# Kernel optimization log

Hardware: AMD Instinct MI355X
Metric: run time of the kernel (lower is better)

Reference implementation:

```python
import jax, jax.numpy as jnp
import numpy as np

MARGIN = 0.3
BIG = jnp.float32(1e30)  # finite sentinel for masked max/min (avoids inf-inf NaNs)


def setup_inputs() -> dict:
    key = jax.random.key(0)
    k1, k2 = jax.random.split(key)
    B, D, N_CLASSES = 8192, 256, 512
    embeddings = jax.random.normal(k1, (B, D), dtype=jnp.float32)
    labels = jax.random.randint(k2, (B,), 0, N_CLASSES, dtype=jnp.int64)
    return {"embeddings": embeddings, "labels": labels}


def reference(embeddings, labels):
    B = embeddings.shape[0]
    # pairwise squared L2 distances via Gram matrix
    dot = embeddings @ embeddings.T                      # [B, B]
    sq = jnp.diagonal(dot)[:, None]                      # [B, 1]
    dist2 = jnp.maximum(sq + sq.T - 2.0 * dot, 0.0)      # [B, B]

    labels_eq = labels[:, None] == labels[None, :]       # [B, B]
    eye = jnp.eye(B, dtype=bool)
    pos_mask = labels_eq & ~eye                          # positives, excluding self
    neg_mask = ~labels_eq

    has_pos = jnp.any(pos_mask, axis=1)                  # rows contributing to loss
    # hardest positive per anchor: masked max
    d_ap = jnp.max(jnp.where(pos_mask, dist2, -BIG), axis=1)  # [B]

    # semi-hard negatives: d_ap < d < d_ap + margin
    semi_hard = neg_mask & (dist2 > d_ap[:, None]) & (dist2 < d_ap[:, None] + MARGIN)
    has_semi = jnp.any(semi_hard, axis=1)
    final_neg = jnp.where(has_semi[:, None], semi_hard, neg_mask)  # fallback to all negatives
    d_an = jnp.min(jnp.where(final_neg, dist2, BIG), axis=1)       # [B]

    per_row = jax.nn.relu(d_ap - d_an + MARGIN)          # [B]
    per_row = jnp.where(has_pos, per_row, 0.0)
    n_valid = jnp.maximum(jnp.sum(has_pos), 1)
    return jnp.sum(per_row) / n_valid.astype(per_row.dtype)
```

## Files before the change

### kernel.cpp

```cpp
#include <hip/hip_runtime.h>

#define MARGIN 0.3f
#define BIGF 1e30f
#define MAXC 64

constexpr int D = 256;

typedef __attribute__((ext_vector_type(8))) _Float16 f16x8;
typedef __attribute__((ext_vector_type(4))) _Float16 f16x4;
typedef __attribute__((ext_vector_type(4))) float f32x4;

__device__ __forceinline__ void gll16(const void* g, void* l) {
  __builtin_amdgcn_global_load_lds(
      (const __attribute__((address_space(1))) unsigned int*)g,
      (__attribute__((address_space(3))) unsigned int*)l, 16, 0, 0);
}

#define SCB() __builtin_amdgcn_sched_barrier(0)
#define BAR() __builtin_amdgcn_s_barrier()
#define WAITV(N) asm volatile("s_waitcnt vmcnt(" #N ")" ::: "memory")

__global__ __launch_bounds__(256)
void k0_prep(const float* __restrict__ E, const int* __restrict__ labels,
             _Float16* __restrict__ H, float* __restrict__ sq,
             unsigned* __restrict__ minAll, unsigned* __restrict__ minAb,
             int* __restrict__ cnt, int* __restrict__ members, int B) {
  int wave = threadIdx.x >> 6, lane = threadIdx.x & 63;
  int row = blockIdx.x * 4 + wave;
  if (row >= B) return;
  float4 v = *(const float4*)&E[(size_t)row * D + lane * 4];
  f16x4 h;
  h.x = (_Float16)v.x; h.y = (_Float16)v.y;
  h.z = (_Float16)v.z; h.w = (_Float16)v.w;
  {
    const int panel = row >> 8, r = row & 255;
    const int kt = lane >> 3;
    const int cc = (lane >> 1) & 3;
    const int slot = cc ^ ((r >> 1) & 3);
    const size_t off = ((size_t)(panel * 8 + kt) * 256 + r) * 32 + slot * 8 + (lane & 1) * 4;
    *(f16x4*)&H[off] = h;
  }
  float s = v.x * v.x + v.y * v.y + v.z * v.z + v.w * v.w;
#pragma unroll
  for (int off = 32; off; off >>= 1) s += __shfl_xor(s, off);
  if (lane == 0) {
    sq[row] = s;
    minAll[row] = __float_as_uint(BIGF);
    minAb[row] = __float_as_uint(BIGF);
    int lab = labels[row];
    int p = atomicAdd(&cnt[lab], 1);
    if (p < MAXC) members[lab * MAXC + p] = row;
  }
}

__global__ __launch_bounds__(256)
void k1_dap(const float* __restrict__ E, const int* __restrict__ labels,
            const float* __restrict__ sq, const int* __restrict__ cnt,
            const int* __restrict__ members, float* __restrict__ d_ap,
            int* __restrict__ haspos, int B) {
  int wave = threadIdx.x >> 6, lane = threadIdx.x & 63;
  int i = blockIdx.x * 4 + wave;
  if (i >= B) return;
  float4 a = *(const float4*)&E[(size_t)i * D + lane * 4];
  int li = labels[i];
  int n = min(cnt[li], MAXC);
  float sqi = sq[i];
  float m = -BIGF;
  const int* mem = &members[li * MAXC];
  int p = 0;
  for (; p + 3 < n; p += 4) {
    int j0 = mem[p], j1 = mem[p + 1], j2 = mem[p + 2], j3 = mem[p + 3];
    float4 b0 = *(const float4*)&E[(size_t)j0 * D + lane * 4];
    float4 b1 = *(const float4*)&E[(size_t)j1 * D + lane * 4];
    float4 b2 = *(const float4*)&E[(size_t)j2 * D + lane * 4];
    float4 b3 = *(const float4*)&E[(size_t)j3 * D + lane * 4];
    float s0 = a.x * b0.x + a.y * b0.y + a.z * b0.z + a.w * b0.w;
    float s1 = a.x * b1.x + a.y * b1.y + a.z * b1.z + a.w * b1.w;
    float s2 = a.x * b2.x + a.y * b2.y + a.z * b2.z + a.w * b2.w;
    float s3 = a.x * b3.x + a.y * b3.y + a.z * b3.z + a.w * b3.w;
#pragma unroll
    for (int off = 32; off; off >>= 1) {
      s0 += __shfl_xor(s0, off);
      s1 += __shfl_xor(s1, off);
      s2 += __shfl_xor(s2, off);
      s3 += __shfl_xor(s3, off);
    }
    float d0 = fmaxf(sqi + sq[j0] - 2.f * s0, 0.f);
    float d1 = fmaxf(sqi + sq[j1] - 2.f * s1, 0.f);
    float d2 = fmaxf(sqi + sq[j2] - 2.f * s2, 0.f);
    float d3 = fmaxf(sqi + sq[j3] - 2.f * s3, 0.f);
    if (j0 != i) m = fmaxf(m, d0);
    if (j1 != i) m = fmaxf(m, d1);
    if (j2 != i) m = fmaxf(m, d2);
    if (j3 != i) m = fmaxf(m, d3);
  }
  for (; p < n; ++p) {
    int j = mem[p];
    if (j == i) continue;
    float4 b = *(const float4*)&E[(size_t)j * D + lane * 4];
    float s = a.x * b.x + a.y * b.y + a.z * b.z + a.w * b.w;
#pragma unroll
    for (int off = 32; off; off >>= 1) s += __shfl_xor(s, off);
    m = fmaxf(m, fmaxf(sqi + sq[j] - 2.f * s, 0.f));
  }
  if (lane == 0) {
    d_ap[i] = (n > 1) ? m : -BIGF;
    haspos[i] = (n > 1) ? 1 : 0;
  }
}

__global__ __launch_bounds__(256, 4)
void k2_f16(const _Float16* __restrict__ H, const float* __restrict__ sq,
            const float* __restrict__ d_ap, const int* __restrict__ labels,
            unsigned* __restrict__ minAll, unsigned* __restrict__ minAb, int T) {
  __shared__ __align__(16) unsigned char smem[32768];
  __shared__ float sqI[128], sqJ[128], dapI[128], dapJ[128];
  __shared__ int labI[128], labJ[128];
  __shared__ unsigned smAJ[128], smBJ[128];

  const int tid = threadIdx.x;
  const int lane = tid & 63;
  const int wave = tid >> 6;
  const int wr = wave >> 1, wc = wave & 1;
  const int lo4 = lane & 15, hi4 = lane >> 4;

  const int nwg = gridDim.x;
  const int bid = blockIdx.x;
  const int swz = ((nwg & 7) == 0) ? (bid & 7) * (nwg >> 3) + (bid >> 3) : bid;
  int ti = (int)((sqrtf(8.f * (float)swz + 1.f) - 1.f) * 0.5f);
  while ((ti + 1) * (ti + 2) / 2 <= swz) ++ti;
  while (ti * (ti + 1) / 2 > swz) --ti;
  const int tj = swz - ti * (ti + 1) / 2;
  const int iBase = ti * 128, jBase = tj * 128;
  const bool offdiag = (ti != tj);

  const _Float16* HA = H + (size_t)(ti >> 1) * 8 * 8192 + (size_t)(ti & 1) * 4096;
  const _Float16* HB = H + (size_t)(tj >> 1) * 8 * 8192 + (size_t)(tj & 1) * 4096;
  const int f0 = tid, f1 = 256 + tid;

  auto STAGE = [&](int buf, int kt) {
    unsigned char* base = smem + buf * 16384;
    const _Float16* sa = HA + (size_t)kt * 8192;
    const _Float16* sb = HB + (size_t)kt * 8192;
    gll16(sa + f0 * 8, base + f0 * 16);
    gll16(sa + f1 * 8, base + f1 * 16);
    gll16(sb + f0 * 8, base + 8192 + f0 * 16);
    gll16(sb + f1 * 8, base + 8192 + f1 * 16);
  };

  f32x4 acc[4][4];
#pragma unroll
  for (int m = 0; m < 4; ++m)
#pragma unroll
    for (int n = 0; n < 4; ++n) acc[m][n] = (f32x4){0.f, 0.f, 0.f, 0.f};

  const int pc = hi4 ^ ((lo4 >> 1) & 3);

  auto COMPUTE = [&](int buf) {
    const _Float16* Ab = (const _Float16*)(smem + buf * 16384);
    const _Float16* Bb = Ab + 4096;
    f16x8 aF[4], bF[4];
#pragma unroll
    for (int m = 0; m < 4; ++m)
      aF[m] = *(const f16x8*)(Ab + (wr * 64 + m * 16 + lo4) * 32 + pc * 8);
#pragma unroll
    for (int n = 0; n < 4; ++n)
      bF[n] = *(const f16x8*)(Bb + (wc * 64 + n * 16 + lo4) * 32 + pc * 8);
    __builtin_amdgcn_s_setprio(1);
#pragma unroll
    for (int m = 0; m < 4; ++m)
#pragma unroll
      for (int n = 0; n < 4; ++n)
        acc[m][n] = __builtin_amdgcn_mfma_f32_16x16x32_f16(aF[m], bF[n], acc[m][n], 0, 0, 0);
    __builtin_amdgcn_s_setprio(0);
  };

  STAGE(0, 0);
  STAGE(1, 1);
  if (tid < 128) {
    int gi = iBase + tid;
    sqI[tid] = sq[gi]; labI[tid] = labels[gi]; dapI[tid] = d_ap[gi];
  } else {
    int t = tid - 128;
    int gj = jBase + t;
    sqJ[t] = sq[gj]; labJ[t] = labels[gj]; dapJ[t] = d_ap[gj];
    smAJ[t] = smBJ[t] = __float_as_uint(BIGF);
  }
  __syncthreads();
  COMPUTE(0); SCB(); BAR(); SCB(); STAGE(0, 2);
  WAITV(4); SCB(); BAR(); SCB(); COMPUTE(1); SCB(); BAR(); SCB(); STAGE(1, 3);
  WAITV(4); SCB(); BAR(); SCB(); COMPUTE(0); SCB(); BAR(); SCB(); STAGE(0, 4);
  WAITV(4); SCB(); BAR(); SCB(); COMPUTE(1); SCB(); BAR(); SCB(); STAGE(1, 5);
  WAITV(4); SCB(); BAR(); SCB(); COMPUTE(0); SCB(); BAR(); SCB(); STAGE(0, 6);
  WAITV(4); SCB(); BAR(); SCB(); COMPUTE(1); SCB(); BAR(); SCB(); STAGE(1, 7);
  WAITV(4); SCB(); BAR(); SCB(); COMPUTE(0); SCB(); BAR(); SCB();
  WAITV(0); SCB(); BAR(); SCB(); COMPUTE(1);
  __syncthreads();

  unsigned* scr = (unsigned*)smem;
#pragma unroll
  for (int s = 0; s < 20; ++s) scr[s * 256 + tid] = 0xFFFFFFFFu;
  __syncthreads();

  float sjv[4], djv[4];
  int ljv[4];
#pragma unroll
  for (int n = 0; n < 4; ++n) {
    int lj = wc * 64 + n * 16 + lo4;
    sjv[n] = sqJ[lj]; djv[n] = dapJ[lj]; ljv[n] = labJ[lj];
  }
  float cA[4], cB[4];
#pragma unroll
  for (int n = 0; n < 4; ++n) { cA[n] = BIGF; cB[n] = BIGF; }

#pragma unroll
  for (int m = 0; m < 4; ++m) {
#pragma unroll
    for (int reg = 0; reg < 4; ++reg) {
      const int li = wr * 64 + m * 16 + hi4 * 4 + reg;
      const float si = sqI[li], da = dapI[li];
      const int lbi = labI[li];
      float rA = BIGF, rB = BIGF;
#pragma unroll
      for (int n = 0; n < 4; ++n) {
        float dd = fmaxf(fmaf(-2.f, acc[m][n][reg], si + sjv[n]), 0.f);
        float ddm = (ljv[n] != lbi) ? dd : BIGF;
        rA = fminf(rA, ddm);
        rB = fminf(rB, (ddm > da) ? ddm : BIGF);
        if (offdiag) {
          cA[n] = fminf(cA[n], ddm);
          cB[n] = fminf(cB[n], (ddm > djv[n]) ? ddm : BIGF);
        }
      }
      atomicMin(&scr[li * 20 + lo4], __float_as_uint(rA));
      atomicMin(&scr[2560 + li * 20 + lo4], __float_as_uint(rB));
    }
  }
  if (offdiag) {
#pragma unroll
    for (int n = 0; n < 4; ++n) {
      const int lj = wc * 64 + n * 16 + lo4;
      float a = cA[n], b = cB[n];
      a = fminf(a, __shfl_xor(a, 16)); b = fminf(b, __shfl_xor(b, 16));
      a = fminf(a, __shfl_xor(a, 32)); b = fminf(b, __shfl_xor(b, 32));
      if (hi4 == 0) {
        atomicMin(&smAJ[lj], __float_as_uint(a));
        atomicMin(&smBJ[lj], __float_as_uint(b));
      }
    }
  }
  __syncthreads();

  {
    const int q = tid >> 7, i = tid & 127;
    const uint4* p4 = (const uint4*)&scr[q * 2560 + i * 20];
    uint4 a = p4[0], b = p4[1], c = p4[2], d4 = p4[3];
    unsigned u = min(min(min(a.x, a.y), min(a.z, a.w)),
                     min(min(min(b.x, b.y), min(b.z, b.w)),
                         min(min(min(c.x, c.y), min(c.z, c.w)),
                             min(min(d4.x, d4.y), min(d4.z, d4.w)))));
    unsigned* dst = q ? minAb : minAll;
    atomicMin(&dst[iBase + i], u);
    if (offdiag) {
      unsigned w = q ? smBJ[i] : smAJ[i];
      atomicMin(&dst[jBase + i], w);
    }
  }
}

__global__ __launch_bounds__(1024)
void k3_final(const float* __restrict__ d_ap, const int* __restrict__ haspos,
              const unsigned* __restrict__ minAll, const unsigned* __restrict__ minAb,
              float* __restrict__ out, int B) {
  __shared__ float ssum[1024];
  __shared__ int scnt[1024];
  int t = threadIdx.x;
  float lsum = 0.f;
  int lcnt = 0;
  for (int i = t; i < B; i += 1024) {
    float mA = __uint_as_float(minAll[i]);
    float mB = __uint_as_float(minAb[i]);
    float dap = d_ap[i];
    float dan = (mB < dap + MARGIN) ? mB : mA;
    float loss = fmaxf(dap - dan + MARGIN, 0.f);
    if (haspos[i]) { lsum += loss; lcnt += 1; }
  }
  ssum[t] = lsum;
  scnt[t] = lcnt;
  __syncthreads();
  for (int off = 512; off; off >>= 1) {
    if (t < off) { ssum[t] += ssum[t + off]; scnt[t] += scnt[t + off]; }
    __syncthreads();
  }
  if (t == 0) out[0] = ssum[0] / (float)max(scnt[0], 1);
}

extern "C" void kernel_launch(void* const* d_in, const int* in_sizes, int n_in,
                              void* d_out, int out_size, void* d_ws, size_t ws_size,
                              hipStream_t stream) {
  const float* E = (const float*)d_in[0];
  const int* labels = (const int*)d_in[1];
  int B = in_sizes[1];

  float* ws = (float*)d_ws;
  float* sq = ws;
  float* dap = ws + B;
  int* haspos = (int*)(ws + 2 * B);
  unsigned* minAll = (unsigned*)(ws + 3 * B);
  unsigned* minAb = (unsigned*)(ws + 4 * B);
  int* cnt = (int*)(ws + 5 * B);
  int* members = cnt + 512;
  _Float16* H = (_Float16*)(members + 512 * MAXC);
  float* out = (float*)d_out;

  hipMemsetAsync(cnt, 0, 512 * sizeof(int), stream);
  k0_prep<<<(B + 3) / 4, 256, 0, stream>>>(E, labels, H, sq, minAll, minAb, cnt, members, B);
  k1_dap<<<(B + 3) / 4, 256, 0, stream>>>(E, labels, sq, cnt, members, dap, haspos, B);
  int T = B / 128;
  int nwg = T * (T + 1) / 2;
  k2_f16<<<nwg, 256, 0, stream>>>(H, sq, dap, labels, minAll, minAb, T);
  k3_final<<<1, 1024, 0, stream>>>(dap, haspos, minAll, minAb, out, B);
}
```

Measured before the change: 78.96 us.

## Replace 4-wave 128x128 Gram tiles with single-wave 64x64 tiles, no barriers

The pairwise-distance kernel now uses one 64-lane wave per workgroup, each handling a 64x64 tile of the upper-triangular Gram matrix instead of four waves sharing a 128x128 tile. With a single wave, all workgroup barriers are removed. Per-row metadata (sq, d_ap, labels) is read straight from global memory, and column minima go directly to global atomics instead of through shared staging. This removes barrier stalls and gives the scheduler many more small workgroups. In exchange, each tile reuses less data, so global fp16 loads and global atomic traffic roughly double.

```diff
diff --git a/kernel.cpp b/kernel.cpp
--- a/kernel.cpp
+++ b/kernel.cpp
@@ -17,8 +17,6 @@
 }
 
 #define SCB() __builtin_amdgcn_sched_barrier(0)
-#define BAR() __builtin_amdgcn_s_barrier()
-#define WAITV(N) asm volatile("s_waitcnt vmcnt(" #N ")" ::: "memory")
 
 __global__ __launch_bounds__(256)
 void k0_prep(const float* __restrict__ E, const int* __restrict__ labels,
@@ -109,19 +107,13 @@
   }
 }
 
-__global__ __launch_bounds__(256, 4)
-void k2_f16(const _Float16* __restrict__ H, const float* __restrict__ sq,
-            const float* __restrict__ d_ap, const int* __restrict__ labels,
-            unsigned* __restrict__ minAll, unsigned* __restrict__ minAb, int T) {
-  __shared__ __align__(16) unsigned char smem[32768];
-  __shared__ float sqI[128], sqJ[128], dapI[128], dapJ[128];
-  __shared__ int labI[128], labJ[128];
-  __shared__ unsigned smAJ[128], smBJ[128];
-
-  const int tid = threadIdx.x;
-  const int lane = tid & 63;
-  const int wave = tid >> 6;
-  const int wr = wave >> 1, wc = wave & 1;
+__global__ __launch_bounds__(64)
+void k2_wave(const _Float16* __restrict__ H, const float* __restrict__ sq,
+             const float* __restrict__ d_ap, const int* __restrict__ labels,
+             unsigned* __restrict__ minAll, unsigned* __restrict__ minAb, int T) {
+  __shared__ __align__(16) _Float16 sm[2][4096];
+
+  const int lane = threadIdx.x;
   const int lo4 = lane & 15, hi4 = lane >> 4;
 
   const int nwg = gridDim.x;
@@ -131,21 +123,22 @@
   while ((ti + 1) * (ti + 2) / 2 <= swz) ++ti;
   while (ti * (ti + 1) / 2 > swz) --ti;
   const int tj = swz - ti * (ti + 1) / 2;
-  const int iBase = ti * 128, jBase = tj * 128;
+  const int iBase = ti * 64, jBase = tj * 64;
   const bool offdiag = (ti != tj);
 
-  const _Float16* HA = H + (size_t)(ti >> 1) * 8 * 8192 + (size_t)(ti & 1) * 4096;
-  const _Float16* HB = H + (size_t)(tj >> 1) * 8 * 8192 + (size_t)(tj & 1) * 4096;
-  const int f0 = tid, f1 = 256 + tid;
+  const _Float16* HA = H + (size_t)(ti >> 2) * 65536 + (size_t)(ti & 3) * 2048;
+  const _Float16* HB = H + (size_t)(tj >> 2) * 65536 + (size_t)(tj & 3) * 2048;
 
   auto STAGE = [&](int buf, int kt) {
-    unsigned char* base = smem + buf * 16384;
     const _Float16* sa = HA + (size_t)kt * 8192;
     const _Float16* sb = HB + (size_t)kt * 8192;
-    gll16(sa + f0 * 8, base + f0 * 16);
-    gll16(sa + f1 * 8, base + f1 * 16);
-    gll16(sb + f0 * 8, base + 8192 + f0 * 16);
-    gll16(sb + f1 * 8, base + 8192 + f1 * 16);
+    _Float16* la = &sm[buf][0] + lane * 8;
+    _Float16* lb = &sm[buf][2048] + lane * 8;
+#pragma unroll
+    for (int p = 0; p < 4; ++p) {
+      gll16(sa + p * 512 + lane * 8, la + p * 512);
+      gll16(sb + p * 512 + lane * 8, lb + p * 512);
+    }
   };
 
   f32x4 acc[4][4];
@@ -155,59 +148,53 @@
     for (int n = 0; n < 4; ++n) acc[m][n] = (f32x4){0.f, 0.f, 0.f, 0.f};
 
   const int pc = hi4 ^ ((lo4 >> 1) & 3);
-
-  auto COMPUTE = [&](int buf) {
-    const _Float16* Ab = (const _Float16*)(smem + buf * 16384);
-    const _Float16* Bb = Ab + 4096;
-    f16x8 aF[4], bF[4];
-#pragma unroll
-    for (int m = 0; m < 4; ++m)
-      aF[m] = *(const f16x8*)(Ab + (wr * 64 + m * 16 + lo4) * 32 + pc * 8);
-#pragma unroll
-    for (int n = 0; n < 4; ++n)
-      bF[n] = *(const f16x8*)(Bb + (wc * 64 + n * 16 + lo4) * 32 + pc * 8);
-    __builtin_amdgcn_s_setprio(1);
-#pragma unroll
-    for (int m = 0; m < 4; ++m)
-#pragma unroll
-      for (int n = 0; n < 4; ++n)
-        acc[m][n] = __builtin_amdgcn_mfma_f32_16x16x32_f16(aF[m], bF[n], acc[m][n], 0, 0, 0);
-    __builtin_amdgcn_s_setprio(0);
-  };
 
   STAGE(0, 0);
   STAGE(1, 1);
-  if (tid < 128) {
-    int gi = iBase + tid;
-    sqI[tid] = sq[gi]; labI[tid] = labels[gi]; dapI[tid] = d_ap[gi];
-  } else {
-    int t = tid - 128;
-    int gj = jBase + t;
-    sqJ[t] = sq[gj]; labJ[t] = labels[gj]; dapJ[t] = d_ap[gj];
-    smAJ[t] = smBJ[t] = __float_as_uint(BIGF);
-  }
-  __syncthreads();
-  COMPUTE(0); SCB(); BAR(); SCB(); STAGE(0, 2);
-  WAITV(4); SCB(); BAR(); SCB(); COMPUTE(1); SCB(); BAR(); SCB(); STAGE(1, 3);
-  WAITV(4); SCB(); BAR(); SCB(); COMPUTE(0); SCB(); BAR(); SCB(); STAGE(0, 4);
-  WAITV(4); SCB(); BAR(); SCB(); COMPUTE(1); SCB(); BAR(); SCB(); STAGE(1, 5);
-  WAITV(4); SCB(); BAR(); SCB(); COMPUTE(0); SCB(); BAR(); SCB(); STAGE(0, 6);
-  WAITV(4); SCB(); BAR(); SCB(); COMPUTE(1); SCB(); BAR(); SCB(); STAGE(1, 7);
-  WAITV(4); SCB(); BAR(); SCB(); COMPUTE(0); SCB(); BAR(); SCB();
-  WAITV(0); SCB(); BAR(); SCB(); COMPUTE(1);
-  __syncthreads();
-
-  unsigned* scr = (unsigned*)smem;
-#pragma unroll
-  for (int s = 0; s < 20; ++s) scr[s * 256 + tid] = 0xFFFFFFFFu;
-  __syncthreads();
+
+#define KSTEP(BUF, NKT, VMW, DOSTAGE)                                          \
+  {                                                                            \
+    asm volatile("s_waitcnt vmcnt(" VMW ")" ::: "memory");                     \
+    SCB();                                                                     \
+    const _Float16* Ab = &sm[BUF][0];                                          \
+    const _Float16* Bb = &sm[BUF][2048];                                       \
+    f16x8 aF[4], bF[4];                                                        \
+    _Pragma("unroll") for (int m = 0; m < 4; ++m)                              \
+        aF[m] = *(const f16x8*)(Ab + (m * 16 + lo4) * 32 + pc * 8);            \
+    _Pragma("unroll") for (int n = 0; n < 4; ++n)                              \
+        bF[n] = *(const f16x8*)(Bb + (n * 16 + lo4) * 32 + pc * 8);            \
+    asm volatile("s_waitcnt lgkmcnt(0)" ::: "memory");                         \
+    SCB();                                                                     \
+    if (DOSTAGE) STAGE(BUF, NKT);                                              \
+    __builtin_amdgcn_s_setprio(1);                                             \
+    _Pragma("unroll") for (int m = 0; m < 4; ++m)                              \
+        _Pragma("unroll") for (int n = 0; n < 4; ++n)                          \
+            acc[m][n] =                                                        \
+                __builtin_amdgcn_mfma_f32_16x16x32_f16(aF[m], bF[n],           \
+                                                       acc[m][n], 0, 0, 0);    \
+    __builtin_amdgcn_s_setprio(0);                                             \
+  }
+
+  KSTEP(0, 2, "8", true);
+  KSTEP(1, 3, "8", true);
+  KSTEP(0, 4, "8", true);
+  KSTEP(1, 5, "8", true);
+  KSTEP(0, 6, "8", true);
+  KSTEP(1, 7, "8", true);
+  KSTEP(0, 0, "8", false);
+  KSTEP(1, 0, "0", false);
+#undef KSTEP
+
+  unsigned* scr = (unsigned*)&sm[0][0];
+#pragma unroll
+  for (int s = 0; s < 40; ++s) scr[s * 64 + lane] = 0xFFFFFFFFu;
 
   float sjv[4], djv[4];
   int ljv[4];
 #pragma unroll
   for (int n = 0; n < 4; ++n) {
-    int lj = wc * 64 + n * 16 + lo4;
-    sjv[n] = sqJ[lj]; djv[n] = dapJ[lj]; ljv[n] = labJ[lj];
+    int gj = jBase + n * 16 + lo4;
+    sjv[n] = sq[gj]; djv[n] = d_ap[gj]; ljv[n] = labels[gj];
   }
   float cA[4], cB[4];
 #pragma unroll
@@ -217,9 +204,9 @@
   for (int m = 0; m < 4; ++m) {
 #pragma unroll
     for (int reg = 0; reg < 4; ++reg) {
-      const int li = wr * 64 + m * 16 + hi4 * 4 + reg;
-      const float si = sqI[li], da = dapI[li];
-      const int lbi = labI[li];
+      const int li = m * 16 + hi4 * 4 + reg;
+      const float si = sq[iBase + li], da = d_ap[iBase + li];
+      const int lbi = labels[iBase + li];
       float rA = BIGF, rB = BIGF;
 #pragma unroll
       for (int n = 0; n < 4; ++n) {
@@ -233,38 +220,34 @@
         }
       }
       atomicMin(&scr[li * 20 + lo4], __float_as_uint(rA));
-      atomicMin(&scr[2560 + li * 20 + lo4], __float_as_uint(rB));
+      atomicMin(&scr[1280 + li * 20 + lo4], __float_as_uint(rB));
     }
   }
   if (offdiag) {
 #pragma unroll
     for (int n = 0; n < 4; ++n) {
-      const int lj = wc * 64 + n * 16 + lo4;
       float a = cA[n], b = cB[n];
       a = fminf(a, __shfl_xor(a, 16)); b = fminf(b, __shfl_xor(b, 16));
       a = fminf(a, __shfl_xor(a, 32)); b = fminf(b, __shfl_xor(b, 32));
       if (hi4 == 0) {
-        atomicMin(&smAJ[lj], __float_as_uint(a));
-        atomicMin(&smBJ[lj], __float_as_uint(b));
+        int gj = jBase + n * 16 + lo4;
+        atomicMin(&minAll[gj], __float_as_uint(a));
+        atomicMin(&minAb[gj], __float_as_uint(b));
       }
     }
   }
-  __syncthreads();
-
-  {
-    const int q = tid >> 7, i = tid & 127;
-    const uint4* p4 = (const uint4*)&scr[q * 2560 + i * 20];
+#pragma unroll
+  for (int it = 0; it < 2; ++it) {
+    const int idx = it * 64 + lane;
+    const int q = idx >> 6, li = idx & 63;
+    const uint4* p4 = (const uint4*)&scr[q * 1280 + li * 20];
     uint4 a = p4[0], b = p4[1], c = p4[2], d4 = p4[3];
     unsigned u = min(min(min(a.x, a.y), min(a.z, a.w)),
                      min(min(min(b.x, b.y), min(b.z, b.w)),
                          min(min(min(c.x, c.y), min(c.z, c.w)),
                              min(min(d4.x, d4.y), min(d4.z, d4.w)))));
     unsigned* dst = q ? minAb : minAll;
-    atomicMin(&dst[iBase + i], u);
-    if (offdiag) {
-      unsigned w = q ? smBJ[i] : smAJ[i];
-      atomicMin(&dst[jBase + i], w);
-    }
+    atomicMin(&dst[iBase + li], u);
   }
 }
 
@@ -316,8 +299,8 @@
   hipMemsetAsync(cnt, 0, 512 * sizeof(int), stream);
   k0_prep<<<(B + 3) / 4, 256, 0, stream>>>(E, labels, H, sq, minAll, minAb, cnt, members, B);
   k1_dap<<<(B + 3) / 4, 256, 0, stream>>>(E, labels, sq, cnt, members, dap, haspos, B);
-  int T = B / 128;
+  int T = B / 64;
   int nwg = T * (T + 1) / 2;
-  k2_f16<<<nwg, 256, 0, stream>>>(H, sq, dap, labels, minAll, minAb, T);
+  k2_wave<<<nwg, 64, 0, stream>>>(H, sq, dap, labels, minAll, minAb, T);
   k3_final<<<1, 1024, 0, stream>>>(dap, haspos, minAll, minAb, out, B);
 }
```

Result: slower. 90.40 us (+14.5%).

## Triple-buffer GEMM staging and fuse final reduction via last-block ticket

Applied to the files above, without the earlier changes.

The k2 tile kernel moves from double to triple-buffered LDS staging with two k-steps of prefetch in flight, and lowers its occupancy hint from 4 to 3 blocks to fit the larger shared memory. The separate single-block final reduction kernel is removed. Its work now runs in whichever k2 block takes the last value of an atomic ticket counter, which saves a kernel launch and its tail. In exchange, every block pays an atomic and a threadfence, there is less occupancy, and the final reduction runs on a 256-thread block instead of 1024 threads.

```diff
diff --git a/kernel.cpp b/kernel.cpp
--- a/kernel.cpp
+++ b/kernel.cpp
@@ -109,14 +109,17 @@
   }
 }
 
-__global__ __launch_bounds__(256, 4)
+__global__ __launch_bounds__(256, 3)
 void k2_f16(const _Float16* __restrict__ H, const float* __restrict__ sq,
             const float* __restrict__ d_ap, const int* __restrict__ labels,
-            unsigned* __restrict__ minAll, unsigned* __restrict__ minAb, int T) {
-  __shared__ __align__(16) unsigned char smem[32768];
+            unsigned* __restrict__ minAll, unsigned* __restrict__ minAb,
+            const int* __restrict__ haspos, unsigned* __restrict__ ticket,
+            float* __restrict__ out, int T, int B) {
+  __shared__ __align__(16) _Float16 stg[3][8192];
   __shared__ float sqI[128], sqJ[128], dapI[128], dapJ[128];
   __shared__ int labI[128], labJ[128];
   __shared__ unsigned smAJ[128], smBJ[128];
+  __shared__ unsigned sdone;
 
   const int tid = threadIdx.x;
   const int lane = tid & 63;
@@ -134,12 +137,12 @@
   const int iBase = ti * 128, jBase = tj * 128;
   const bool offdiag = (ti != tj);
 
-  const _Float16* HA = H + (size_t)(ti >> 1) * 8 * 8192 + (size_t)(ti & 1) * 4096;
-  const _Float16* HB = H + (size_t)(tj >> 1) * 8 * 8192 + (size_t)(tj & 1) * 4096;
+  const _Float16* HA = H + (size_t)(ti >> 1) * 65536 + (size_t)(ti & 1) * 4096;
+  const _Float16* HB = H + (size_t)(tj >> 1) * 65536 + (size_t)(tj & 1) * 4096;
   const int f0 = tid, f1 = 256 + tid;
 
   auto STAGE = [&](int buf, int kt) {
-    unsigned char* base = smem + buf * 16384;
+    unsigned char* base = (unsigned char*)&stg[buf][0];
     const _Float16* sa = HA + (size_t)kt * 8192;
     const _Float16* sb = HB + (size_t)kt * 8192;
     gll16(sa + f0 * 8, base + f0 * 16);
@@ -157,7 +160,7 @@
   const int pc = hi4 ^ ((lo4 >> 1) & 3);
 
   auto COMPUTE = [&](int buf) {
-    const _Float16* Ab = (const _Float16*)(smem + buf * 16384);
+    const _Float16* Ab = &stg[buf][0];
     const _Float16* Bb = Ab + 4096;
     f16x8 aF[4], bF[4];
 #pragma unroll
@@ -177,6 +180,7 @@
 
   STAGE(0, 0);
   STAGE(1, 1);
+  STAGE(2, 2);
   if (tid < 128) {
     int gi = iBase + tid;
     sqI[tid] = sq[gi]; labI[tid] = labels[gi]; dapI[tid] = d_ap[gi];
@@ -187,17 +191,18 @@
     smAJ[t] = smBJ[t] = __float_as_uint(BIGF);
   }
   __syncthreads();
-  COMPUTE(0); SCB(); BAR(); SCB(); STAGE(0, 2);
-  WAITV(4); SCB(); BAR(); SCB(); COMPUTE(1); SCB(); BAR(); SCB(); STAGE(1, 3);
-  WAITV(4); SCB(); BAR(); SCB(); COMPUTE(0); SCB(); BAR(); SCB(); STAGE(0, 4);
-  WAITV(4); SCB(); BAR(); SCB(); COMPUTE(1); SCB(); BAR(); SCB(); STAGE(1, 5);
-  WAITV(4); SCB(); BAR(); SCB(); COMPUTE(0); SCB(); BAR(); SCB(); STAGE(0, 6);
-  WAITV(4); SCB(); BAR(); SCB(); COMPUTE(1); SCB(); BAR(); SCB(); STAGE(1, 7);
-  WAITV(4); SCB(); BAR(); SCB(); COMPUTE(0); SCB(); BAR(); SCB();
-  WAITV(0); SCB(); BAR(); SCB(); COMPUTE(1);
-  __syncthreads();
-
-  unsigned* scr = (unsigned*)smem;
+
+  COMPUTE(0); SCB(); BAR(); SCB(); STAGE(0, 3); WAITV(8); SCB(); BAR(); SCB();
+  COMPUTE(1); SCB(); BAR(); SCB(); STAGE(1, 4); WAITV(8); SCB(); BAR(); SCB();
+  COMPUTE(2); SCB(); BAR(); SCB(); STAGE(2, 5); WAITV(8); SCB(); BAR(); SCB();
+  COMPUTE(0); SCB(); BAR(); SCB(); STAGE(0, 6); WAITV(8); SCB(); BAR(); SCB();
+  COMPUTE(1); SCB(); BAR(); SCB(); STAGE(1, 7); WAITV(8); SCB(); BAR(); SCB();
+  COMPUTE(2); SCB(); BAR(); SCB(); WAITV(4); SCB(); BAR(); SCB();
+  COMPUTE(0); SCB(); BAR(); SCB(); WAITV(0); SCB(); BAR(); SCB();
+  COMPUTE(1);
+  __syncthreads();
+
+  unsigned* scr = (unsigned*)&stg[0][0];
 #pragma unroll
   for (int s = 0; s < 20; ++s) scr[s * 256 + tid] = 0xFFFFFFFFu;
   __syncthreads();
@@ -266,33 +271,38 @@
       atomicMin(&dst[jBase + i], w);
     }
   }
-}
-
-__global__ __launch_bounds__(1024)
-void k3_final(const float* __restrict__ d_ap, const int* __restrict__ haspos,
-              const unsigned* __restrict__ minAll, const unsigned* __restrict__ minAb,
-              float* __restrict__ out, int B) {
-  __shared__ float ssum[1024];
-  __shared__ int scnt[1024];
-  int t = threadIdx.x;
-  float lsum = 0.f;
-  int lcnt = 0;
-  for (int i = t; i < B; i += 1024) {
-    float mA = __uint_as_float(minAll[i]);
-    float mB = __uint_as_float(minAb[i]);
-    float dap = d_ap[i];
-    float dan = (mB < dap + MARGIN) ? mB : mA;
-    float loss = fmaxf(dap - dan + MARGIN, 0.f);
-    if (haspos[i]) { lsum += loss; lcnt += 1; }
-  }
-  ssum[t] = lsum;
-  scnt[t] = lcnt;
-  __syncthreads();
-  for (int off = 512; off; off >>= 1) {
-    if (t < off) { ssum[t] += ssum[t + off]; scnt[t] += scnt[t + off]; }
+
+  __syncthreads();
+  if (tid == 0) {
+    __threadfence();
+    sdone = atomicAdd(ticket, 1u);
+  }
+  __syncthreads();
+  if (sdone == (unsigned)(nwg - 1)) {
+    __threadfence();
+    float* rsum = (float*)&stg[2][0];
+    int* rcnt = (int*)(rsum + 256);
+    float lsum = 0.f;
+    int lcnt = 0;
+    for (int i = tid; i < B; i += 256) {
+      unsigned uA = atomicMin(&minAll[i], 0xFFFFFFFFu);
+      unsigned uB = atomicMin(&minAb[i], 0xFFFFFFFFu);
+      float mA = __uint_as_float(uA);
+      float mB = __uint_as_float(uB);
+      float dap = d_ap[i];
+      float dan = (mB < dap + MARGIN) ? mB : mA;
+      float loss = fmaxf(dap - dan + MARGIN, 0.f);
+      if (haspos[i]) { lsum += loss; lcnt += 1; }
+    }
+    rsum[tid] = lsum;
+    rcnt[tid] = lcnt;
     __syncthreads();
-  }
-  if (t == 0) out[0] = ssum[0] / (float)max(scnt[0], 1);
+    for (int off = 128; off; off >>= 1) {
+      if (tid < off) { rsum[tid] += rsum[tid + off]; rcnt[tid] += rcnt[tid + off]; }
+      __syncthreads();
+    }
+    if (tid == 0) out[0] = rsum[0] / (float)max(rcnt[0], 1);
+  }
 }
 
 extern "C" void kernel_launch(void* const* d_in, const int* in_sizes, int n_in,
@@ -309,15 +319,15 @@
   unsigned* minAll = (unsigned*)(ws + 3 * B);
   unsigned* minAb = (unsigned*)(ws + 4 * B);
   int* cnt = (int*)(ws + 5 * B);
-  int* members = cnt + 512;
+  unsigned* ticket = (unsigned*)(cnt + 512);
+  int* members = cnt + 516;
   _Float16* H = (_Float16*)(members + 512 * MAXC);
   float* out = (float*)d_out;
 
-  hipMemsetAsync(cnt, 0, 512 * sizeof(int), stream);
+  hipMemsetAsync(cnt, 0, 516 * sizeof(int), stream);
   k0_prep<<<(B + 3) / 4, 256, 0, stream>>>(E, labels, H, sq, minAll, minAb, cnt, members, B);
   k1_dap<<<(B + 3) / 4, 256, 0, stream>>>(E, labels, sq, cnt, members, dap, haspos, B);
   int T = B / 128;
   int nwg = T * (T + 1) / 2;
-  k2_f16<<<nwg, 256, 0, stream>>>(H, sq, dap, labels, minAll, minAb, T);
-  k3_final<<<1, 1024, 0, stream>>>(dap, haspos, minAll, minAb, out, B);
-}
+  k2_f16<<<nwg, 256, 0, stream>>>(H, sq, dap, labels, minAll, minAb, haspos, ticket, out, T, B);
+}
```

After: 113.9 us. +44.3%, slower.
